# Performance work log

Hardware: AMD Instinct MI355X
Metric: run time of the kernel (lower is better)

Reference implementation:

```python
import jax, jax.numpy as jnp
import numpy as np

# ---- layer config (yolov3, layer_no=2) ----
STRIDE = 8
N_CLASSES = 80
IGNORE_TH = 0.7
ANCHORS_PX = np.array([[10,13],[16,30],[33,23],[30,61],[62,45],[59,119],[116,90],[156,198],[373,326]], np.float32)
ALL_ANCHORS = ANCHORS_PX / STRIDE          # [9,2] in grid units
ANCHOR_ID_LO, ANCHOR_ID_HI = 0, 2          # anchor_mask[2] = [0,1,2]
ANCHORS = ALL_ANCHORS[ANCHOR_ID_LO:ANCHOR_ID_HI+1]  # [3,2]
NA = 3
NC = N_CLASSES + 5

B, IN_CH, NG, NBOX = 16, 256, 76, 50


def _safe_log(p):
    # emulate torch BCE's log clamp at -100; eps stops 0*inf -> nan
    return jnp.maximum(jnp.log(jnp.maximum(p, 1e-12)), -100.0)


def _bce_sum(p, t, w=None):
    l = -(t * _safe_log(p) + (1.0 - t) * _safe_log(1.0 - p))
    if w is not None:
        l = l * w
    return l.sum()


def setup_inputs() -> dict:
    key = jax.random.key(0)
    k1, k2, k3, k4, k5 = jax.random.split(key, 5)
    xin = jax.random.normal(k1, (B, IN_CH, NG, NG), jnp.float32)
    cls = jax.random.randint(k2, (B, NBOX, 1), 0, N_CLASSES).astype(jnp.float32)
    cxy = jax.random.uniform(k3, (B, NBOX, 2), jnp.float32, 0.02, 0.98)
    wh = jax.random.uniform(k4, (B, NBOX, 2), jnp.float32, 0.02, 0.40)
    labels = jnp.concatenate([cls, cxy, wh], axis=-1)  # [B,N,5]
    W = jax.random.normal(k5, (NA * NC, IN_CH), jnp.float32) * 0.02  # 1x1 conv
    b = jnp.zeros((NA * NC,), jnp.float32)
    return {"xin": xin, "labels": labels, "W": W, "b": b}


def _yolo_loss(xin, labels, W, b):
    nB, _, nG, _ = xin.shape
    anchors = jnp.asarray(ANCHORS, xin.dtype)          # [3,2]
    all_anchors = jnp.asarray(ALL_ANCHORS, xin.dtype)  # [9,2]

    # 1x1 conv -> [B, A, G, G, C]
    x = jnp.einsum('bchw,oc->bohw', xin, W) + b[None, :, None, None]
    x = x.reshape(nB, NA, NC, nG, nG).transpose(0, 1, 3, 4, 2)

    xy = jax.nn.sigmoid(x[..., :2])
    wh = x[..., 2:4]
    conf_cls = jax.nn.sigmoid(x[..., 4:])  # [B,A,G,G,1+ncls]

    gy, gx = jnp.meshgrid(jnp.arange(nG, dtype=x.dtype), jnp.arange(nG, dtype=x.dtype), indexing='ij')
    pred_boxes = jnp.stack([
        xy[..., 0] + gx,
        xy[..., 1] + gy,
        jnp.exp(wh[..., 0]) * anchors[:, 0][None, :, None, None],
        jnp.exp(wh[..., 1]) * anchors[:, 1][None, :, None, None]], axis=-1)  # [B,A,G,G,4]

    # ---- ground truth ----
    valid = labels.sum(-1) > 0                     # [B,N]
    gt_cls = labels[..., 0].astype(jnp.int32)
    gt = labels[..., 1:] * nG                      # [B,N,4] cx,cy,w,h in grid units
    gt_x, gt_y, gt_w, gt_h = gt[..., 0], gt[..., 1], gt[..., 2], gt[..., 3]
    gi = jnp.floor(gt_x).astype(jnp.int32)
    gj = jnp.floor(gt_y).astype(jnp.int32)

    # best anchor per gt: wh-IoU vs all 9 anchors (centered at origin)
    inter_a = jnp.minimum(gt_w[..., None], all_anchors[:, 0]) * jnp.minimum(gt_h[..., None], all_anchors[:, 1])
    union_a = gt_w[..., None] * gt_h[..., None] + all_anchors[:, 0] * all_anchors[:, 1] - inter_a
    best = jnp.argmax(inter_a / union_a, axis=-1)  # [B,N]
    in_mask = (best >= ANCHOR_ID_LO) & (best <= ANCHOR_ID_HI)
    a = jnp.where(in_mask, best % 3, -1)           # [B,N]

    # all-pairs IoU: pred boxes vs gt boxes (ignore mask)
    pb = pred_boxes.reshape(nB, -1, 4)             # [B,M,4], M = A*G*G
    pa_area = pb[..., 2] * pb[..., 3]
    gt_area = gt_w * gt_h
    tl = jnp.maximum(pb[:, :, None, :2] - pb[:, :, None, 2:] / 2, gt[:, None, :, :2] - gt[:, None, :, 2:] / 2)
    br = jnp.minimum(pb[:, :, None, :2] + pb[:, :, None, 2:] / 2, gt[:, None, :, :2] + gt[:, None, :, 2:] / 2)
    inter = jnp.prod(br - tl, -1) * jnp.all(tl < br, -1)
    iou = inter / (pa_area[:, :, None] + gt_area[:, None, :] - inter)
    iou = jnp.where(valid[:, None, :], iou, 0.0)
    best_iou = iou.max(-1)                         # [B,M]
    has_boxes = valid.any(-1)
    obj_mask = jnp.where(has_boxes[:, None], best_iou <= IGNORE_TH, True).reshape(nB, NA, nG, nG)

    # ---- scatter target assignment ----
    assign = valid & (a >= 0)
    a_safe = jnp.clip(a, 0, NA - 1)
    aw = anchors[a_safe, 0]
    ah = anchors[a_safe, 1]
    tvec = jnp.concatenate([
        (gt_x - jnp.floor(gt_x))[..., None],
        (gt_y - jnp.floor(gt_y))[..., None],
        jnp.log(gt_w / aw + 1e-16)[..., None],
        jnp.log(gt_h / ah + 1e-16)[..., None],
        jnp.ones_like(gt_x)[..., None],
        jax.nn.one_hot(gt_cls, N_CLASSES, dtype=x.dtype)], axis=-1)  # [B,N,NC]
    sval = 2.0 - gt_w * gt_h / (nG * nG)

    bf = jnp.broadcast_to(jnp.arange(nB)[:, None], a.shape).reshape(-1)
    af = jnp.where(assign, a_safe, NA).reshape(-1)  # NA is OOB -> dropped
    jf = gj.reshape(-1)
    if_ = gi.reshape(-1)

    target = jnp.zeros((nB, NA, nG, nG, NC), x.dtype).at[bf, af, jf, if_].set(tvec.reshape(-1, NC), mode='drop')
    scale = jnp.zeros((nB, NA, nG, nG), x.dtype).at[bf, af, jf, if_].set(sval.reshape(-1), mode='drop')
    obj_mask = obj_mask.at[bf, af, jf, if_].set(True, mode='drop')
    noobj = jnp.zeros((nB, NA, nG, nG), bool).at[bf, af, jf, if_].set(True, mode='drop')

    # ---- losses ----
    nm = noobj.astype(x.dtype)[..., None]
    p_obj = conf_cls[..., 0] * obj_mask
    t_obj = target[..., 4] * obj_mask
    p_xy = xy * nm
    t_xy = target[..., :2] * nm
    p_wh = wh * nm
    t_wh = target[..., 2:4] * nm
    p_cls = conf_cls[..., 1:] * nm
    t_cls = target[..., 5:] * nm
    sc = scale[..., None]

    loss_xy = _bce_sum(p_xy, t_xy, sc)
    rs = jnp.sqrt(sc)
    loss_wh = 0.5 * jnp.sum((p_wh * rs - t_wh * rs) ** 2)
    loss_obj = _bce_sum(p_obj, t_obj)
    loss_cls = _bce_sum(p_cls, t_cls)
    loss = loss_xy + loss_wh + loss_obj + loss_cls
    return jnp.stack([loss, loss_xy, loss_wh, loss_obj, loss_cls])


def reference(xin, labels, W, b):
    return _yolo_loss(xin, labels, W, b)
```

## Files before the change

### kernel.cpp

```cpp
#include <hip/hip_runtime.h>
#include <math.h>

#define NB    16
#define NAg   3
#define NCg   85
#define NCLS  80
#define NGg   76
#define NSp   (NGg*NGg)
#define NG4   (NSp/4)
#define NCELL (NAg*NSp)
#define NBOX  50
#define INCH  256

#define ACC_OFF  0
#define WIN_OFF  32
#define GD_OFF   (WIN_OFF + NB*NCELL*4)
#define GI_OFF   (GD_OFF + NB*NBOX*10*4)
#define PART_OFF (GI_OFF + NB*NBOX*2*4)
#define PART_SZ1 ((size_t)NB*15*NSp*4)
#define NEED4    (PART_OFF + 4*PART_SZ1)
#define ZERO_BYTES GD_OFF

__device__ __constant__ float c_AW[9] = {1.25f,2.0f,4.125f,3.75f,7.75f,7.375f,14.5f,19.5f,46.625f};
__device__ __constant__ float c_AH[9] = {1.625f,3.75f,2.875f,7.625f,5.625f,14.875f,11.25f,24.75f,40.75f};

__device__ __forceinline__ float safe_log(float p) {
    return fmaxf(logf(fmaxf(p, 1e-12f)), -100.0f);
}
__device__ __forceinline__ float sigm(float x) {
    return 1.0f / (1.0f + expf(-x));
}

template<int NSLICE>
__global__ __launch_bounds__(128) void k_gemm_part(
    const float* __restrict__ xin, const float* __restrict__ W,
    float* __restrict__ part)
{
    constexpr int CPS = INCH / NSLICE;
    const int g  = blockIdx.x * 128 + threadIdx.x;
    if (g >= NG4) return;
    const int b  = blockIdx.y;
    const int sl = blockIdx.z;
    const int s0 = g * 4;

    float4 acc[15];
#pragma unroll
    for (int f = 0; f < 15; f++) acc[f] = make_float4(0.f,0.f,0.f,0.f);

    const float* xp = xin + ((size_t)b * INCH + sl * CPS) * NSp + s0;
    const float* wp = W + sl * CPS;

#pragma unroll
    for (int cc = 0; cc < CPS; cc += 16) {
        float4 xv[16];
#pragma unroll
        for (int i = 0; i < 16; i++)
            xv[i] = *(const float4*)(xp + (size_t)(cc + i) * NSp);
#pragma unroll
        for (int i = 0; i < 16; i++) {
#pragma unroll
            for (int f = 0; f < 15; f++) {
                const int row = (f / 5) * NCg + (f % 5);
                const float w = wp[row * INCH + cc + i];
                acc[f].x += w * xv[i].x; acc[f].y += w * xv[i].y;
                acc[f].z += w * xv[i].z; acc[f].w += w * xv[i].w;
            }
        }
    }
#pragma unroll
    for (int f = 0; f < 15; f++)
        *(float4*)&part[(((size_t)sl * NB + b) * 15 + f) * NSp + s0] = acc[f];
}

__global__ void k_labels(const float* __restrict__ labels,
                         float* __restrict__ gdata, int* __restrict__ gint,
                         int* __restrict__ win)
{
    int t = blockIdx.x * blockDim.x + threadIdx.x;
    if (t >= NB * NBOX) return;
    int b = t / NBOX, n = t % NBOX;

    const float* L = labels + (size_t)t * 5;
    float l0 = L[0], l1 = L[1], l2 = L[2], l3 = L[3], l4 = L[4];
    int valid = (l0 + l1 + l2 + l3 + l4) > 0.f;

    float gx = l1 * NGg, gy = l2 * NGg, gw = l3 * NGg, gh = l4 * NGg;

    int best = 0; float brr = -1.f;
#pragma unroll
    for (int k = 0; k < 9; k++) {
        float inter = fminf(gw, c_AW[k]) * fminf(gh, c_AH[k]);
        float uni   = gw*gh + c_AW[k]*c_AH[k] - inter;
        float r     = inter / uni;
        if (r > brr) { brr = r; best = k; }
    }
    int a = (best <= 2) ? best : -1;
    int assign = valid && (a >= 0);
    int a_safe = a < 0 ? 0 : (a > 2 ? 2 : a);

    float* gd = gdata + (size_t)t * 10;
    gd[0] = gx; gd[1] = gy; gd[2] = gw; gd[3] = gh;
    gd[4] = gx - floorf(gx);
    gd[5] = gy - floorf(gy);
    gd[6] = logf(gw / c_AW[a_safe] + 1e-16f);
    gd[7] = logf(gh / c_AH[a_safe] + 1e-16f);
    gd[8] = 2.f - gw * gh / (float)NSp;
    gd[9] = valid ? 1.f : 0.f;

    int gi = (int)floorf(gx), gj = (int)floorf(gy);
    int inb = (gi >= 0) && (gi < NGg) && (gj >= 0) && (gj < NGg);
    int cell = (assign && inb) ? (a * NSp + gj * NGg + gi) : -1;
    gint[t*2 + 0] = cell;
    gint[t*2 + 1] = (int)l0;

    if (cell >= 0) atomicMax(&win[b * NCELL + cell], n + 1);
}

template<int NSLICE>
__global__ __launch_bounds__(256) void k_fuse(
    const float* __restrict__ part, const float* __restrict__ bias,
    const float* __restrict__ gdata, const int* __restrict__ win,
    float* __restrict__ acc)
{
    __shared__ float sb[NBOX][5];
    __shared__ int sHas;
    __shared__ float red[256];

    const int b = blockIdx.y;
    const int tid = threadIdx.x;

    if (tid < NBOX) {
        const float* gd = gdata + ((size_t)b * NBOX + tid) * 10;
        sb[tid][0] = gd[0]; sb[tid][1] = gd[1];
        sb[tid][2] = gd[2]; sb[tid][3] = gd[3];
        sb[tid][4] = gd[9];
    }
    if (tid == 0) sHas = 0;
    __syncthreads();
    if (tid < NBOX && sb[tid][4] > 0.f) atomicOr(&sHas, 1);
    __syncthreads();

    const int cell = blockIdx.x * 256 + tid;
    float l = 0.f;
    if (cell < NCELL) {
        const int a = cell / NSp, s = cell % NSp;
        float x0 = 0.f, x1 = 0.f, x2 = 0.f, x3 = 0.f, x4 = 0.f;
#pragma unroll
        for (int sl = 0; sl < NSLICE; sl++) {
            const float* pp = part + (((size_t)sl * NB + b) * 15 + a * 5) * NSp + s;
            x0 += pp[0*NSp]; x1 += pp[1*NSp]; x2 += pp[2*NSp];
            x3 += pp[3*NSp]; x4 += pp[4*NSp];
        }
        const float gxf = (float)(s % NGg);
        const float gyf = (float)(s / NGg);
        float px = sigm(x0 + bias[a*NCg+0]) + gxf;
        float py = sigm(x1 + bias[a*NCg+1]) + gyf;
        float pw = expf(x2 + bias[a*NCg+2]) * c_AW[a];
        float ph = expf(x3 + bias[a*NCg+3]) * c_AH[a];
        float cf = sigm(x4 + bias[a*NCg+4]);
        float pa = pw * ph;
        float bi = 0.f;
        for (int n = 0; n < NBOX; n++) {
            if (sb[n][4] > 0.f) {
                float gx = sb[n][0], gy = sb[n][1], gw = sb[n][2], gh = sb[n][3];
                float tlx = fmaxf(px - pw*0.5f, gx - gw*0.5f);
                float tly = fmaxf(py - ph*0.5f, gy - gh*0.5f);
                float brx = fminf(px + pw*0.5f, gx + gw*0.5f);
                float bry = fminf(py + ph*0.5f, gy + gh*0.5f);
                float inter = ((tlx < brx) && (tly < bry)) ? (brx-tlx)*(bry-tly) : 0.f;
                float iou = inter / (pa + gw*gh - inter);
                bi = fmaxf(bi, iou);
            }
        }
        bool maskpre  = sHas ? (bi <= 0.7f) : true;
        bool assigned = win[b * NCELL + cell] > 0;
        if (maskpre || assigned) {
            float t = assigned ? 1.f : 0.f;
            l = -(t * safe_log(cf) + (1.f - t) * safe_log(1.f - cf));
        }
    }
    red[tid] = l;
    __syncthreads();
    for (int o = 128; o > 0; o >>= 1) {
        if (tid < o) red[tid] += red[tid + o];
        __syncthreads();
    }
    if (tid == 0) atomicAdd(&acc[2], red[0]);
}

__global__ __launch_bounds__(256) void k_assigned(
    const float* __restrict__ xin, const float* __restrict__ W,
    const float* __restrict__ bias, const float* __restrict__ gdata,
    const int* __restrict__ gint, const int* __restrict__ win,
    float* __restrict__ acc)
{
    const int t = blockIdx.x;
    const int b = t / NBOX, n = t % NBOX;
    const int cell = gint[t*2];
    if (cell < 0) return;
    if (win[b * NCELL + cell] != n + 1) return;

    const int a = cell / NSp, s = cell % NSp;
    const int o0 = a * NCg;
    const int tid = threadIdx.x;

    __shared__ float4 col4[64];
    __shared__ float  xsh[NCg];
    __shared__ float  sacc[3];

    ((float*)col4)[tid] = xin[((size_t)b * INCH + tid) * NSp + s];
    if (tid < 3) sacc[tid] = 0.f;
    __syncthreads();

    const int wid = tid >> 6, lane = tid & 63;
    for (int o = wid; o < NCg; o += 4) {
        const float4 wv = *(const float4*)&W[(size_t)(o0 + o) * INCH + lane * 4];
        const float4 cv = col4[lane];
        float p = wv.x*cv.x + wv.y*cv.y + wv.z*cv.z + wv.w*cv.w;
        for (int off = 32; off; off >>= 1) p += __shfl_down(p, off);
        if (lane == 0) xsh[o] = p + bias[o0 + o];
    }
    __syncthreads();

    if (tid < NCg) {
        const float* gd = gdata + (size_t)t * 10;
        const float sval = gd[8];
        const int gcls = gint[t*2 + 1];
        float val = xsh[tid];
        float term; int slot;
        if (tid < 2) {
            float tgt = gd[4 + tid];
            float p = sigm(val);
            term = -(tgt * safe_log(p) + (1.f - tgt) * safe_log(1.f - p)) * sval;
            slot = 0;
        } else if (tid < 4) {
            float tgt = gd[4 + tid];
            float d = val - tgt;
            term = 0.5f * sval * d * d;
            slot = 1;
        } else if (tid == 4) {
            term = 0.f; slot = 2;
        } else {
            float tgt = ((tid - 5) == gcls) ? 1.f : 0.f;
            float p = sigm(val);
            term = -(tgt * safe_log(p) + (1.f - tgt) * safe_log(1.f - p));
            slot = 2;
        }
        atomicAdd(&sacc[slot], term);
    }
    __syncthreads();
    if (tid == 0) {
        atomicAdd(&acc[0], sacc[0]);
        atomicAdd(&acc[1], sacc[1]);
        atomicAdd(&acc[3], sacc[2]);
    }
}

__global__ void k_final(const float* __restrict__ acc, float* __restrict__ out)
{
    float xy = acc[0], wh = acc[1], ob = acc[2], cl = acc[3];
    out[0] = xy + wh + ob + cl;
    out[1] = xy; out[2] = wh; out[3] = ob; out[4] = cl;
}

extern "C" void kernel_launch(void* const* d_in, const int* in_sizes, int n_in,
                              void* d_out, int out_size, void* d_ws, size_t ws_size,
                              hipStream_t stream)
{
    const float* xin    = (const float*)d_in[0];
    const float* labels = (const float*)d_in[1];
    const float* W      = (const float*)d_in[2];
    const float* bias   = (const float*)d_in[3];

    char* ws = (char*)d_ws;
    float* acc   = (float*)(ws + ACC_OFF);
    int*   win   = (int*)  (ws + WIN_OFF);
    float* gdata = (float*)(ws + GD_OFF);
    int*   gint  = (int*)  (ws + GI_OFF);
    float* part  = (float*)(ws + PART_OFF);
    float* out   = (float*)d_out;

    const bool big = (ws_size >= (size_t)NEED4);

    hipMemsetAsync(ws, 0, ZERO_BYTES, stream);

    k_labels<<<dim3((NB*NBOX + 255)/256), 256, 0, stream>>>(labels, gdata, gint, win);

    const int gx = (NG4 + 127) / 128;
    if (big) k_gemm_part<4><<<dim3(gx, NB, 4), 128, 0, stream>>>(xin, W, part);
    else     k_gemm_part<1><<<dim3(gx, NB, 1), 128, 0, stream>>>(xin, W, part);

    const int fx = (NCELL + 255) / 256;
    if (big) k_fuse<4><<<dim3(fx, NB), 256, 0, stream>>>(part, bias, gdata, win, acc);
    else     k_fuse<1><<<dim3(fx, NB), 256, 0, stream>>>(part, bias, gdata, win, acc);

    k_assigned<<<dim3(NB*NBOX), 256, 0, stream>>>(xin, W, bias, gdata, gint, win, acc);
    k_final<<<1, 1, 0, stream>>>(acc, out);
}
```

Measured before the change: 242.8 us.

## Replace split-K register GEMM with LDS-tiled double-buffered single-pass GEMM

The head-channel projection drops its four-way channel split and its partial-sum buffers. Each block now stages the 15 needed weight rows in shared memory and streams 16-channel chunks of the input through a double-buffered shared tile. This cuts partial-sum writes and the re-reads in the fuse kernel, and removes the workspace-size branch. The cost is fewer blocks in flight (368 blocks instead of 768) and more shared-memory traffic and barriers per block, which could lower memory-level parallelism on a bandwidth-bound pass.

New measurement: 260.0 us. 1.07x slower.

```diff
diff --git a/kernel.cpp b/kernel.cpp
--- a/kernel.cpp
+++ b/kernel.cpp
@@ -7,22 +7,22 @@
 #define NCLS  80
 #define NGg   76
 #define NSp   (NGg*NGg)
-#define NG4   (NSp/4)
 #define NCELL (NAg*NSp)
 #define NBOX  50
 #define INCH  256
+#define CHUNK 16
+#define NTILE 23
 
 #define ACC_OFF  0
 #define WIN_OFF  32
 #define GD_OFF   (WIN_OFF + NB*NCELL*4)
 #define GI_OFF   (GD_OFF + NB*NBOX*10*4)
 #define PART_OFF (GI_OFF + NB*NBOX*2*4)
-#define PART_SZ1 ((size_t)NB*15*NSp*4)
-#define NEED4    (PART_OFF + 4*PART_SZ1)
 #define ZERO_BYTES GD_OFF
 
 __device__ __constant__ float c_AW[9] = {1.25f,2.0f,4.125f,3.75f,7.75f,7.375f,14.5f,19.5f,46.625f};
 __device__ __constant__ float c_AH[9] = {1.625f,3.75f,2.875f,7.625f,5.625f,14.875f,11.25f,24.75f,40.75f};
+__device__ __constant__ int   c_ROW[15] = {0,1,2,3,4, 85,86,87,88,89, 170,171,172,173,174};
 
 __device__ __forceinline__ float safe_log(float p) {
     return fmaxf(logf(fmaxf(p, 1e-12f)), -100.0f);
@@ -31,45 +31,76 @@
     return 1.0f / (1.0f + expf(-x));
 }
 
-template<int NSLICE>
-__global__ __launch_bounds__(128) void k_gemm_part(
+__global__ __launch_bounds__(256) void k_gemm_lds(
     const float* __restrict__ xin, const float* __restrict__ W,
     float* __restrict__ part)
 {
-    constexpr int CPS = INCH / NSLICE;
-    const int g  = blockIdx.x * 128 + threadIdx.x;
-    if (g >= NG4) return;
-    const int b  = blockIdx.y;
-    const int sl = blockIdx.z;
-    const int s0 = g * 4;
-
-    float4 acc[15];
-#pragma unroll
-    for (int f = 0; f < 15; f++) acc[f] = make_float4(0.f,0.f,0.f,0.f);
-
-    const float* xp = xin + ((size_t)b * INCH + sl * CPS) * NSp + s0;
-    const float* wp = W + sl * CPS;
-
-#pragma unroll
-    for (int cc = 0; cc < CPS; cc += 16) {
-        float4 xv[16];
-#pragma unroll
-        for (int i = 0; i < 16; i++)
-            xv[i] = *(const float4*)(xp + (size_t)(cc + i) * NSp);
-#pragma unroll
-        for (int i = 0; i < 16; i++) {
+    __shared__ float wsm[15][256];
+    __shared__ float xs[2][CHUNK][256];
+
+    const int tid = threadIdx.x;
+    const int b   = blockIdx.y;
+    const int sp0 = blockIdx.x * 256;
+
+    for (int idx = tid; idx < 15 * 256; idx += 256) {
+        const int f = idx >> 8, c = idx & 255;
+        wsm[f][c] = W[(size_t)c_ROW[f] * INCH + c];
+    }
+
+    const int lsp = (tid & 63) * 4;
+    const int lch = tid >> 6;
+    int spl = sp0 + lsp;
+    if (spl > NSp - 4) spl = NSp - 4;
+    const float* xb = xin + (size_t)b * INCH * NSp + spl;
+
+    float4 xv[4];
+#pragma unroll
+    for (int i = 0; i < 4; i++)
+        xv[i] = *(const float4*)(xb + (size_t)(lch + 4*i) * NSp);
+    __syncthreads();
+#pragma unroll
+    for (int i = 0; i < 4; i++)
+        *(float4*)&xs[0][lch + 4*i][lsp] = xv[i];
+
+    float acc[15];
+#pragma unroll
+    for (int f = 0; f < 15; f++) acc[f] = 0.f;
+
+    for (int k = 0; k < INCH / CHUNK; k++) {
+        const int buf = k & 1;
+        if (k + 1 < INCH / CHUNK) {
+            const int c0 = (k + 1) * CHUNK;
+#pragma unroll
+            for (int i = 0; i < 4; i++)
+                xv[i] = *(const float4*)(xb + (size_t)(c0 + lch + 4*i) * NSp);
+        }
+        __syncthreads();
+        if (k + 1 < INCH / CHUNK) {
+#pragma unroll
+            for (int i = 0; i < 4; i++)
+                *(float4*)&xs[buf ^ 1][lch + 4*i][lsp] = xv[i];
+        }
+        const int cb = k * CHUNK;
+#pragma unroll
+        for (int cg = 0; cg < CHUNK; cg += 4) {
+            const float x0 = xs[buf][cg+0][tid];
+            const float x1 = xs[buf][cg+1][tid];
+            const float x2 = xs[buf][cg+2][tid];
+            const float x3 = xs[buf][cg+3][tid];
 #pragma unroll
             for (int f = 0; f < 15; f++) {
-                const int row = (f / 5) * NCg + (f % 5);
-                const float w = wp[row * INCH + cc + i];
-                acc[f].x += w * xv[i].x; acc[f].y += w * xv[i].y;
-                acc[f].z += w * xv[i].z; acc[f].w += w * xv[i].w;
+                const float4 wv = *(const float4*)&wsm[f][cb + cg];
+                acc[f] += wv.x*x0 + wv.y*x1 + wv.z*x2 + wv.w*x3;
             }
         }
     }
-#pragma unroll
-    for (int f = 0; f < 15; f++)
-        *(float4*)&part[(((size_t)sl * NB + b) * 15 + f) * NSp + s0] = acc[f];
+
+    const int s = sp0 + tid;
+    if (s < NSp) {
+#pragma unroll
+        for (int f = 0; f < 15; f++)
+            part[((size_t)b * 15 + f) * NSp + s] = acc[f];
+    }
 }
 
 __global__ void k_labels(const float* __restrict__ labels,
@@ -116,7 +147,6 @@
     if (cell >= 0) atomicMax(&win[b * NCELL + cell], n + 1);
 }
 
-template<int NSLICE>
 __global__ __launch_bounds__(256) void k_fuse(
     const float* __restrict__ part, const float* __restrict__ bias,
     const float* __restrict__ gdata, const int* __restrict__ win,
@@ -144,13 +174,9 @@
     float l = 0.f;
     if (cell < NCELL) {
         const int a = cell / NSp, s = cell % NSp;
-        float x0 = 0.f, x1 = 0.f, x2 = 0.f, x3 = 0.f, x4 = 0.f;
-#pragma unroll
-        for (int sl = 0; sl < NSLICE; sl++) {
-            const float* pp = part + (((size_t)sl * NB + b) * 15 + a * 5) * NSp + s;
-            x0 += pp[0*NSp]; x1 += pp[1*NSp]; x2 += pp[2*NSp];
-            x3 += pp[3*NSp]; x4 += pp[4*NSp];
-        }
+        const float* pp = part + ((size_t)b * 15 + a * 5) * NSp + s;
+        float x0 = pp[0*NSp], x1 = pp[1*NSp], x2 = pp[2*NSp];
+        float x3 = pp[3*NSp], x4 = pp[4*NSp];
         const float gxf = (float)(s % NGg);
         const float gyf = (float)(s / NGg);
         float px = sigm(x0 + bias[a*NCg+0]) + gxf;
@@ -280,20 +306,11 @@
     float* part  = (float*)(ws + PART_OFF);
     float* out   = (float*)d_out;
 
-    const bool big = (ws_size >= (size_t)NEED4);
-
     hipMemsetAsync(ws, 0, ZERO_BYTES, stream);
 
-    k_labels<<<dim3((NB*NBOX + 255)/256), 256, 0, stream>>>(labels, gdata, gint, win);
-
-    const int gx = (NG4 + 127) / 128;
-    if (big) k_gemm_part<4><<<dim3(gx, NB, 4), 128, 0, stream>>>(xin, W, part);
-    else     k_gemm_part<1><<<dim3(gx, NB, 1), 128, 0, stream>>>(xin, W, part);
-
-    const int fx = (NCELL + 255) / 256;
-    if (big) k_fuse<4><<<dim3(fx, NB), 256, 0, stream>>>(part, bias, gdata, win, acc);
-    else     k_fuse<1><<<dim3(fx, NB), 256, 0, stream>>>(part, bias, gdata, win, acc);
-
+    k_labels  <<<dim3((NB*NBOX + 255)/256), 256, 0, stream>>>(labels, gdata, gint, win);
+    k_gemm_lds<<<dim3(NTILE, NB), 256, 0, stream>>>(xin, W, part);
+    k_fuse    <<<dim3((NCELL + 255)/256, NB), 256, 0, stream>>>(part, bias, gdata, win, acc);
     k_assigned<<<dim3(NB*NBOX), 256, 0, stream>>>(xin, W, bias, gdata, gint, win, acc);
-    k_final<<<1, 1, 0, stream>>>(acc, out);
-}
+    k_final   <<<1, 1, 0, stream>>>(acc, out);
+}
```
